# Performance work log

Measured on AMD Instinct MI355X. Metric: run time of the kernel, lower is better.

## Reference

```python
import jax, jax.numpy as jnp
import numpy as np
from jax import lax

EPS = 1e-10
ALPHA = 1000.0

def _gauss_kernel(k=3, mu=0.0, sigma=3.0):
    g1 = np.linspace(-1.0, 1.0, k)
    x, y = np.meshgrid(g1, g1)
    d = np.sqrt(x ** 2 + y ** 2)
    g = np.exp(-(d - mu) ** 2 / (2.0 * sigma ** 2)) / (2.0 * np.pi * sigma ** 2)
    return jnp.asarray(g / g.sum(), jnp.float32)

def _sobel_kernel(k=3, transpose=False):
    r = np.linspace(-(k // 2), k // 2, k)
    x, y = np.meshgrid(r, r)
    den = x ** 2 + y ** 2
    den[:, k // 2] = 1.0
    s = x / den
    if transpose:
        s = s.T
    return jnp.asarray(s, jnp.float32)

def _canny_nms_kernels():
    # 8 directional difference kernels (center minus neighbor), E, SE, S, SW, W, NW, N, NE
    off = [(1, 2), (2, 2), (2, 1), (2, 0), (1, 0), (0, 0), (0, 1), (0, 2)]
    k = np.zeros((8, 3, 3), np.float32)
    k[:, 1, 1] = 1.0
    for i, (r, c) in enumerate(off):
        k[i, r, c] = -1.0
    return jnp.asarray(k)

def _dwconv_reflect(x, k2d):
    # depthwise 3x3 conv with reflect padding (same as padding_mode='reflect', groups=C)
    C = x.shape[1]
    xp = jnp.pad(x, ((0, 0), (0, 0), (1, 1), (1, 1)), mode='reflect')
    w = jnp.broadcast_to(k2d[None, None], (C, 1, 3, 3))
    return lax.conv_general_dilated(xp, w, (1, 1), 'VALID', feature_group_count=C)

def _forward(x, w_expand, w_perm_gauss, w_perm_sx, w_perm_sy, w_merge, low_t, high_t):
    gauss = _gauss_kernel(3, 0.0, 3.0)
    sob_x = _sobel_kernel(3, transpose=False)
    sob_y = _sobel_kernel(3, transpose=True)
    canny = _canny_nms_kernels()  # (8,3,3)
    # 1x1 channel expansion
    h = jnp.einsum('oc,bchw->bohw', w_expand, x)
    # gaussian blur (depthwise) + trainable 1x1 permute
    g = jnp.einsum('oc,bchw->bohw', w_perm_gauss, _dwconv_reflect(h, gauss))
    gx = jnp.einsum('oc,bchw->bohw', w_perm_sx, _dwconv_reflect(g, sob_x))
    gy = jnp.einsum('oc,bchw->bohw', w_perm_sy, _dwconv_reflect(g, sob_y))
    mag = jnp.sqrt(gx * gx + gy * gy + EPS)  # (B,C,H,W)
    # NMSConv2d: every output kernel applies the same directional diff summed over ALL input
    # channels, so the 8C outputs repeat with period 8 -> compute 8 dirs on the channel-sum.
    s = jnp.sum(mag, axis=1, keepdims=True)  # (B,1,H,W)
    dirs = lax.conv_general_dilated(s, canny[:, None], (1, 1), [(1, 1), (1, 1)])  # (B,8,H,W)
    deg = jnp.arctan2(gy, gx) * (180.0 / np.pi)
    idx = jnp.mod(jnp.round(deg / 45.0), 8.0).astype(jnp.int32)  # (B,C,H,W) in [0,8)
    pos = jnp.take_along_axis(dirs[:, None], idx[:, :, None], axis=2)[:, :, 0]
    neg = jnp.take_along_axis(dirs[:, None], ((idx + 4) % 8)[:, :, None], axis=2)[:, :, 0]
    nms = mag * ((pos > 0) & (neg > 0)).astype(mag.dtype)
    # soft double threshold (steep sigmoids)
    strong = jax.nn.sigmoid(ALPHA * (nms - high_t))
    weak = 0.5 * (jax.nn.sigmoid(ALPHA * (high_t - nms)) - jax.nn.sigmoid(ALPHA * (low_t - nms)))
    thr = weak + strong
    # merge C -> 1
    m = jnp.einsum('oc,bchw->bohw', w_merge, thr)  # (B,1,H,W)
    # one-step hysteresis: strong pixels promote neighbouring weak (==0.5) pixels
    img_strong = jnp.where(m == 1.0, m, 0.0)
    masked = (m == 0.5)
    hyst = _dwconv_reflect(img_strong, jnp.full((3, 3), 1.25, m.dtype))
    changed = jnp.where((hyst > 1.0) & masked, m, 0.0) + img_strong
    return changed

def setup_inputs() -> dict:
    key = jax.random.key(0)
    k0, k1, k2 = jax.random.split(key, 3)
    B, Cin, C, H, W = 8, 3, 8, 512, 512
    x = jax.random.uniform(k0, (B, Cin, H, W), jnp.float32)
    w_expand = jax.nn.softmax(jax.random.uniform(k1, (C, Cin), jnp.float32), axis=0)
    eye = jnp.eye(C, dtype=jnp.float32)
    bound = 1.0 / np.sqrt(C)
    w_merge = jax.random.uniform(k2, (1, C), jnp.float32, minval=-bound, maxval=bound)
    low_t = jnp.full((C, 1, 1), 0.1, jnp.float32)
    high_t = jnp.full((C, 1, 1), 0.2, jnp.float32)
    return {'x': x, 'w_expand': w_expand, 'w_perm_gauss': eye, 'w_perm_sx': eye,
            'w_perm_sy': eye, 'w_merge': w_merge, 'low_t': low_t, 'high_t': high_t}

def reference(x, w_expand, w_perm_gauss, w_perm_sx, w_perm_sy, w_merge, low_t, high_t):
    return _forward(x, w_expand, w_perm_gauss, w_perm_sx, w_perm_sy, w_merge, low_t, high_t)
```

## Files before the change

kernel.cpp:

```cpp
#include <hip/hip_runtime.h>
#include <math.h>

#define Bsz 8
#define HWp (512*512)
#define TS 32
#define SG 36
#define MG 34
#define XW 40
#define BW 38
#define NT 512
#define K2E 1442.6950408889634f

#if __has_builtin(__builtin_amdgcn_exp2f)
#define EXP2F(x) __builtin_amdgcn_exp2f(x)
#else
#define EXP2F(x) __expf(0.6931471805599453f*(x))
#endif

__device__ __forceinline__ int refl(int i, int n) {
    i = (i < 0) ? -i : i;
    return (i >= n) ? (2*n - 2 - i) : i;
}

__global__ void k_mats(const float* __restrict__ we, const float* __restrict__ pg,
                       const float* __restrict__ psx, const float* __restrict__ psy,
                       const float* __restrict__ wm, const float* __restrict__ lowt,
                       const float* __restrict__ hight, float* __restrict__ mats) {
    if (threadIdx.x == 0 && blockIdx.x == 0) {
        float M1[8][3];
        for (int o = 0; o < 8; ++o)
            for (int c = 0; c < 3; ++c) {
                float a = 0.f;
                for (int k = 0; k < 8; ++k) a += pg[o*8+k] * we[k*3+c];
                M1[o][c] = a;
            }
        for (int o = 0; o < 8; ++o)
            for (int c = 0; c < 3; ++c) {
                float a = 0.f, b = 0.f;
                for (int k = 0; k < 8; ++k) { a += psx[o*8+k]*M1[k][c]; b += psy[o*8+k]*M1[k][c]; }
                mats[o*3+c]      = a;
                mats[24 + o*3+c] = b;
            }
        for (int o = 0; o < 8; ++o) {
            mats[48+o] = hight[o] * K2E;
            mats[56+o] = lowt[o]  * K2E;
            mats[64+o] = 0.5f * wm[o];
        }
    }
}

__global__ __launch_bounds__(NT) void k_fused(
    const float* __restrict__ x, const float* __restrict__ mats,
    float* __restrict__ out, float wc, float wE, float wk)
{
    __shared__ float sm1[3*XW*XW];
    __shared__ float blb[3*BW*BW];

    const int b  = blockIdx.z;
    const int x0 = blockIdx.x*TS, y0 = blockIdx.y*TS;
    const int t  = threadIdx.x;
    const bool inter = (blockIdx.x > 0) && ((int)blockIdx.x < (int)gridDim.x-1) &&
                       (blockIdx.y > 0) && ((int)blockIdx.y < (int)gridDim.y-1);

    const float* xb = x + (size_t)b*3*HWp;

    if (inter) {
        const float* xo = xb + (size_t)(y0-4)*512 + (x0-4);
        for (int i = t; i < 3*XW*10; i += NT) {
            int c = i/400; int j = i - c*400; int r = j/10; int q = j - r*10;
            float4 v = *(const float4*)(xo + (size_t)c*HWp + r*512 + q*4);
            *(float4*)&sm1[c*(XW*XW) + r*XW + q*4] = v;
        }
    } else {
        for (int i = t; i < XW*XW; i += NT) {
            int r = i/XW, cc = i - r*XW;
            size_t off = (size_t)refl(y0-4+r,512)*512 + refl(x0-4+cc,512);
            #pragma unroll
            for (int c = 0; c < 3; ++c)
                sm1[c*(XW*XW)+i] = xb[(size_t)c*HWp + off];
        }
    }
    __syncthreads();

    if (inter) {
        for (int i = t; i < BW*BW; i += NT) {
            int r = i/BW, cc = i - r*BW;
            const int base = (r+1)*XW + (cc+1);
            #pragma unroll
            for (int c = 0; c < 3; ++c) {
                const float* xp = &sm1[c*(XW*XW) + base];
                blb[c*(BW*BW)+i] =
                    wk*(xp[-XW-1]+xp[-XW+1]+xp[XW-1]+xp[XW+1]) +
                    wE*(xp[-XW]+xp[-1]+xp[1]+xp[XW]) + wc*xp[0];
            }
        }
    } else {
        for (int i = t; i < BW*BW; i += NT) {
            int r = i/BW, cc = i - r*BW;
            int iy = refl(y0-3+r,512) - (y0-4);
            int ix = refl(x0-3+cc,512) - (x0-4);
            const int base = iy*XW + ix;
            #pragma unroll
            for (int c = 0; c < 3; ++c) {
                const float* xp = &sm1[c*(XW*XW) + base];
                blb[c*(BW*BW)+i] =
                    wk*(xp[-XW-1]+xp[-XW+1]+xp[XW-1]+xp[XW+1]) +
                    wE*(xp[-XW]+xp[-1]+xp[1]+xp[XW]) + wc*xp[0];
            }
        }
    }
    __syncthreads();

    float mg[3][8];
    unsigned qk[3];
    #pragma unroll
    for (int it = 0; it < 3; ++it) {
        int i = t + it*NT;
        qk[it] = 0;
        if (i < SG*SG) {
            int r = i/SG, cc = i - r*SG;
            float txv[3], tyv[3];
            #pragma unroll
            for (int c = 0; c < 3; ++c) {
                const float* bp = &blb[c*(BW*BW) + r*BW + cc];
                float v00=bp[0],    v01=bp[1],      v02=bp[2];
                float v10=bp[BW],                   v12=bp[BW+2];
                float v20=bp[2*BW], v21=bp[2*BW+1], v22=bp[2*BW+2];
                txv[c] = 0.5f*(v02-v00) + (v12-v10) + 0.5f*(v22-v20);
                tyv[c] = 0.5f*(v20-v00) + (v21-v01) + 0.5f*(v22-v02);
            }
            float s = 0.f; unsigned pk = 0;
            #pragma unroll
            for (int o = 0; o < 8; ++o) {
                float gx  = mats[o*3]*txv[0]    + mats[o*3+1]*txv[1]    + mats[o*3+2]*txv[2];
                float gy  = mats[24+o*3]*tyv[0] + mats[24+o*3+1]*tyv[1] + mats[24+o*3+2]*tyv[2];
                float mgv = __builtin_amdgcn_sqrtf(gx*gx + gy*gy + 1e-10f);
                mg[it][o] = mgv; s += mgv;
                float ax = fabsf(gx), ay = fabsf(gy);
                unsigned qo;
                if (ay <= 0.41421356237309503f*ax)      qo = 0u;
                else if (ax <= 0.41421356237309503f*ay) qo = 2u;
                else qo = ((gx >= 0.f) == (gy >= 0.f)) ? 1u : 3u;
                pk |= qo << (2*o);
            }
            qk[it] = pk;
            #pragma unroll
            for (int o = 0; o < 8; ++o) { asm volatile("" : "+v"(mg[it][o])); }
            asm volatile("" : "+v"(qk[it]));
            int gy_ = y0-2+r, gx_ = x0-2+cc;
            bool inimg = ((unsigned)gy_ < 512u) && ((unsigned)gx_ < 512u);
            sm1[i] = inimg ? s : 0.f;
        }
    }
    __syncthreads();

    {
        float* sS = sm1;
        float* mS = sm1 + SG*SG;
        const float* hiK = mats + 48;
        const float* loK = mats + 56;
        const float* wmh = mats + 64;
        #pragma unroll
        for (int it = 0; it < 3; ++it) {
            int i = t + it*NT;
            if (i < SG*SG) {
                int r = i/SG, cc = i - r*SG;
                if (r >= 1 && r < SG-1 && cc >= 1 && cc < SG-1) {
                    const float* sp = &sS[i];
                    float sc = sp[0];
                    unsigned mask = 0;
                    mask |= ((sc > sp[1])    && (sc > sp[-1]))    ? 1u : 0u;
                    mask |= ((sc > sp[SG+1]) && (sc > sp[-SG-1])) ? 2u : 0u;
                    mask |= ((sc > sp[SG])   && (sc > sp[-SG]))   ? 4u : 0u;
                    mask |= ((sc > sp[SG-1]) && (sc > sp[-SG+1])) ? 8u : 0u;
                    unsigned pk = qk[it];
                    float m = 0.f;
                    #pragma unroll
                    for (int o = 0; o < 8; ++o) {
                        float nms = ((mask >> ((pk >> (2*o)) & 3u)) & 1u) ? mg[it][o] : 0.f;
                        float shi = __builtin_amdgcn_rcpf(1.f + EXP2F(fmaf(nms, -K2E, hiK[o])));
                        float slo = __builtin_amdgcn_rcpf(1.f + EXP2F(fmaf(nms, -K2E, loK[o])));
                        m += wmh[o]*(shi + slo);
                    }
                    mS[(r-1)*MG + (cc-1)] = m;
                }
            }
        }
    }
    __syncthreads();

    {
        const float* mS = sm1 + SG*SG;
        for (int i2 = t; i2 < TS*TS; i2 += NT) {
            int ty_ = i2/TS, tx_ = i2 - ty_*TS;
            int y = y0 + ty_, xg = x0 + tx_;
            const float* mp = &mS[(ty_+1)*MG + (tx_+1)];
            float mc = mp[0];
            float hy = 0.f;
            if (inter) {
                #pragma unroll
                for (int dy = -1; dy <= 1; ++dy)
                    #pragma unroll
                    for (int dx = -1; dx <= 1; ++dx)
                        hy += (mp[dy*MG+dx] == 1.0f) ? 1.25f : 0.f;
            } else {
                #pragma unroll
                for (int dy = -1; dy <= 1; ++dy)
                    #pragma unroll
                    for (int dx = -1; dx <= 1; ++dx) {
                        int ly = refl(y+dy,512) - (y0-1);
                        int lx = refl(xg+dx,512) - (x0-1);
                        hy += (mS[ly*MG+lx] == 1.0f) ? 1.25f : 0.f;
                    }
            }
            float strong = (mc == 1.0f) ? mc : 0.f;
            out[(size_t)b*HWp + (size_t)y*512 + xg] =
                (((hy > 1.0f) && (mc == 0.5f)) ? mc : 0.f) + strong;
        }
    }
}

extern "C" void kernel_launch(void* const* d_in, const int* in_sizes, int n_in,
                              void* d_out, int out_size, void* d_ws, size_t ws_size,
                              hipStream_t stream) {
    const float* x    = (const float*)d_in[0];
    const float* we   = (const float*)d_in[1];
    const float* pg   = (const float*)d_in[2];
    const float* psx  = (const float*)d_in[3];
    const float* psy  = (const float*)d_in[4];
    const float* wm   = (const float*)d_in[5];
    const float* lowt = (const float*)d_in[6];
    const float* hit  = (const float*)d_in[7];
    float* mats = (float*)d_ws;
    float* outp = (float*)d_out;

    double e1 = exp(-1.0/18.0), e2 = exp(-2.0/18.0);
    double sum = 1.0 + 4.0*e1 + 4.0*e2;
    float wc = (float)(1.0/sum), wE = (float)(e1/sum), wk = (float)(e2/sum);

    k_mats<<<1, 64, 0, stream>>>(we, pg, psx, psy, wm, lowt, hit, mats);
    k_fused<<<dim3(512/TS, 512/TS, Bsz), dim3(NT), 0, stream>>>(
        x, mats, outp, wc, wE, wk);
}
```

Baseline: 53.54 us.

## Use column-strip sliding windows for blur/Sobel and skip tiles without strong pixels

Result: faster. 52.43 us (-2.1%).

```diff
diff --git a/kernel.cpp b/kernel.cpp
--- a/kernel.cpp
+++ b/kernel.cpp
@@ -10,6 +10,7 @@
 #define BW 38
 #define NT 512
 #define K2E 1442.6950408889634f
+#define T2q 0.17157287525380993f
 
 #if __has_builtin(__builtin_amdgcn_exp2f)
 #define EXP2F(x) __builtin_amdgcn_exp2f(x)
@@ -55,12 +56,15 @@
 {
     __shared__ float sm1[3*XW*XW];
     __shared__ float blb[3*BW*BW];
+    __shared__ int anyS;
 
     const int b  = blockIdx.z;
     const int x0 = blockIdx.x*TS, y0 = blockIdx.y*TS;
     const int t  = threadIdx.x;
     const bool inter = (blockIdx.x > 0) && ((int)blockIdx.x < (int)gridDim.x-1) &&
                        (blockIdx.y > 0) && ((int)blockIdx.y < (int)gridDim.y-1);
+
+    if (t == 0) anyS = 0;
 
     const float* xb = x + (size_t)b*3*HWp;
 
@@ -83,15 +87,25 @@
     __syncthreads();
 
     if (inter) {
-        for (int i = t; i < BW*BW; i += NT) {
-            int r = i/BW, cc = i - r*BW;
-            const int base = (r+1)*XW + (cc+1);
-            #pragma unroll
-            for (int c = 0; c < 3; ++c) {
-                const float* xp = &sm1[c*(XW*XW) + base];
-                blb[c*(BW*BW)+i] =
-                    wk*(xp[-XW-1]+xp[-XW+1]+xp[XW-1]+xp[XW+1]) +
-                    wE*(xp[-XW]+xp[-1]+xp[1]+xp[XW]) + wc*xp[0];
+        if (t < 494) {
+            int g = t/38, cb = t - g*38, r0 = 3*g;
+            #pragma unroll
+            for (int c = 0; c < 3; ++c) {
+                const float* col = &sm1[c*(XW*XW) + cb];
+                float* bo = &blb[c*(BW*BW) + cb];
+                float a0 = col[r0*XW],     a1 = col[r0*XW+1],     a2 = col[r0*XW+2];
+                float e0 = col[(r0+1)*XW], e1 = col[(r0+1)*XW+1], e2 = col[(r0+1)*XW+2];
+                #pragma unroll
+                for (int ir = 0; ir < 3; ++ir) {
+                    int r = r0 + ir;
+                    if (r < BW) {
+                        float f0 = col[(r+2)*XW], f1 = col[(r+2)*XW+1], f2 = col[(r+2)*XW+2];
+                        float t0 = a0+f0, t1 = a1+f1, t2 = a2+f2;
+                        float u = t0+t2, v = e0+e2, w = t1+v;
+                        bo[r*BW] = wk*u + wE*w + wc*e1;
+                        a0=e0; a1=e1; a2=e2; e0=f0; e1=f1; e2=f2;
+                    }
+                }
             }
         }
     } else {
@@ -113,76 +127,83 @@
 
     float mg[3][8];
     unsigned qk[3];
-    #pragma unroll
-    for (int it = 0; it < 3; ++it) {
-        int i = t + it*NT;
-        qk[it] = 0;
-        if (i < SG*SG) {
-            int r = i/SG, cc = i - r*SG;
-            float txv[3], tyv[3];
-            #pragma unroll
-            for (int c = 0; c < 3; ++c) {
-                const float* bp = &blb[c*(BW*BW) + r*BW + cc];
-                float v00=bp[0],    v01=bp[1],      v02=bp[2];
-                float v10=bp[BW],                   v12=bp[BW+2];
-                float v20=bp[2*BW], v21=bp[2*BW+1], v22=bp[2*BW+2];
-                txv[c] = 0.5f*(v02-v00) + (v12-v10) + 0.5f*(v22-v20);
-                tyv[c] = 0.5f*(v20-v00) + (v21-v01) + 0.5f*(v22-v02);
-            }
+    const int gC = t/36, csC = t - gC*36, r0C = 3*gC;
+    const bool actC = (t < 432);
+    if (actC) {
+        float txv[3][3], tyv[3][3];
+        #pragma unroll
+        for (int c = 0; c < 3; ++c) {
+            const float* blc = &blb[c*(BW*BW) + csC];
+            float p0 = blc[r0C*BW],     p1 = blc[r0C*BW+1],     p2 = blc[r0C*BW+2];
+            float q0 = blc[(r0C+1)*BW], q1 = blc[(r0C+1)*BW+1], q2 = blc[(r0C+1)*BW+2];
+            float D0 = p2-p0, E0 = fmaf(0.5f, p0+p2, p1);
+            float D1 = q2-q0, E1 = fmaf(0.5f, q0+q2, q1);
+            #pragma unroll
+            for (int ir = 0; ir < 3; ++ir) {
+                const float* wr = &blc[(r0C+2+ir)*BW];
+                float w0 = wr[0], w1 = wr[1], w2 = wr[2];
+                float D2 = w2-w0, E2 = fmaf(0.5f, w0+w2, w1);
+                txv[ir][c] = fmaf(0.5f, D0+D2, D1);
+                tyv[ir][c] = E2 - E0;
+                D0 = D1; D1 = D2; E0 = E1; E1 = E2;
+            }
+        }
+        #pragma unroll
+        for (int ir = 0; ir < 3; ++ir) {
             float s = 0.f; unsigned pk = 0;
             #pragma unroll
             for (int o = 0; o < 8; ++o) {
-                float gx  = mats[o*3]*txv[0]    + mats[o*3+1]*txv[1]    + mats[o*3+2]*txv[2];
-                float gy  = mats[24+o*3]*tyv[0] + mats[24+o*3+1]*tyv[1] + mats[24+o*3+2]*tyv[2];
-                float mgv = __builtin_amdgcn_sqrtf(gx*gx + gy*gy + 1e-10f);
-                mg[it][o] = mgv; s += mgv;
-                float ax = fabsf(gx), ay = fabsf(gy);
-                unsigned qo;
-                if (ay <= 0.41421356237309503f*ax)      qo = 0u;
-                else if (ax <= 0.41421356237309503f*ay) qo = 2u;
-                else qo = ((gx >= 0.f) == (gy >= 0.f)) ? 1u : 3u;
+                float gx = mats[o*3]*txv[ir][0]    + mats[o*3+1]*txv[ir][1]    + mats[o*3+2]*txv[ir][2];
+                float gy = mats[24+o*3]*tyv[ir][0] + mats[24+o*3+1]*tyv[ir][1] + mats[24+o*3+2]*tyv[ir][2];
+                float gx2 = gx*gx, gy2 = gy*gy;
+                float mag = __builtin_amdgcn_sqrtf(gx2 + gy2 + 1e-10f);
+                mg[ir][o] = mag; s += mag;
+                unsigned dv = 1u | (((__float_as_uint(gx) ^ __float_as_uint(gy)) >> 30) & 2u);
+                unsigned qo = (gx2 <= T2q*gy2) ? 2u : dv;
+                qo = (gy2 <= T2q*gx2) ? 0u : qo;
                 pk |= qo << (2*o);
             }
-            qk[it] = pk;
-            #pragma unroll
-            for (int o = 0; o < 8; ++o) { asm volatile("" : "+v"(mg[it][o])); }
-            asm volatile("" : "+v"(qk[it]));
-            int gy_ = y0-2+r, gx_ = x0-2+cc;
+            qk[ir] = pk;
+            #pragma unroll
+            for (int o = 0; o < 8; ++o) { asm volatile("" : "+v"(mg[ir][o])); }
+            asm volatile("" : "+v"(qk[ir]));
+            int rr = r0C + ir;
+            int gy_ = y0-2+rr, gx_ = x0-2+csC;
             bool inimg = ((unsigned)gy_ < 512u) && ((unsigned)gx_ < 512u);
-            sm1[i] = inimg ? s : 0.f;
+            sm1[rr*SG + csC] = inimg ? s : 0.f;
         }
     }
     __syncthreads();
 
     {
-        float* sS = sm1;
+        const float* sS = sm1;
         float* mS = sm1 + SG*SG;
         const float* hiK = mats + 48;
         const float* loK = mats + 56;
         const float* wmh = mats + 64;
-        #pragma unroll
-        for (int it = 0; it < 3; ++it) {
-            int i = t + it*NT;
-            if (i < SG*SG) {
-                int r = i/SG, cc = i - r*SG;
-                if (r >= 1 && r < SG-1 && cc >= 1 && cc < SG-1) {
-                    const float* sp = &sS[i];
+        if (actC && csC >= 1 && csC <= 34) {
+            #pragma unroll
+            for (int ir = 0; ir < 3; ++ir) {
+                int r = r0C + ir;
+                if (r >= 1 && r <= 34) {
+                    const float* sp = &sS[r*SG + csC];
                     float sc = sp[0];
                     unsigned mask = 0;
                     mask |= ((sc > sp[1])    && (sc > sp[-1]))    ? 1u : 0u;
                     mask |= ((sc > sp[SG+1]) && (sc > sp[-SG-1])) ? 2u : 0u;
                     mask |= ((sc > sp[SG])   && (sc > sp[-SG]))   ? 4u : 0u;
                     mask |= ((sc > sp[SG-1]) && (sc > sp[-SG+1])) ? 8u : 0u;
-                    unsigned pk = qk[it];
+                    unsigned pk = qk[ir];
                     float m = 0.f;
                     #pragma unroll
                     for (int o = 0; o < 8; ++o) {
-                        float nms = ((mask >> ((pk >> (2*o)) & 3u)) & 1u) ? mg[it][o] : 0.f;
+                        float nms = ((mask >> ((pk >> (2*o)) & 3u)) & 1u) ? mg[ir][o] : 0.f;
                         float shi = __builtin_amdgcn_rcpf(1.f + EXP2F(fmaf(nms, -K2E, hiK[o])));
                         float slo = __builtin_amdgcn_rcpf(1.f + EXP2F(fmaf(nms, -K2E, loK[o])));
                         m += wmh[o]*(shi + slo);
                     }
-                    mS[(r-1)*MG + (cc-1)] = m;
+                    mS[(r-1)*MG + (csC-1)] = m;
+                    if (m == 1.0f) anyS = 1;
                 }
             }
         }
@@ -191,31 +212,40 @@
 
     {
         const float* mS = sm1 + SG*SG;
-        for (int i2 = t; i2 < TS*TS; i2 += NT) {
-            int ty_ = i2/TS, tx_ = i2 - ty_*TS;
-            int y = y0 + ty_, xg = x0 + tx_;
-            const float* mp = &mS[(ty_+1)*MG + (tx_+1)];
-            float mc = mp[0];
-            float hy = 0.f;
-            if (inter) {
-                #pragma unroll
-                for (int dy = -1; dy <= 1; ++dy)
+        float* op = out + (size_t)b*HWp;
+        if (anyS == 0) {
+            #pragma unroll
+            for (int i2 = t; i2 < TS*TS; i2 += NT) {
+                int ty_ = i2>>5, tx_ = i2&31;
+                op[(size_t)(y0+ty_)*512 + (x0+tx_)] = 0.f;
+            }
+        } else {
+            for (int i2 = t; i2 < TS*TS; i2 += NT) {
+                int ty_ = i2>>5, tx_ = i2&31;
+                int y = y0 + ty_, xg = x0 + tx_;
+                const float* mp = &mS[(ty_+1)*MG + (tx_+1)];
+                float mc = mp[0];
+                float hy = 0.f;
+                if (inter) {
                     #pragma unroll
-                    for (int dx = -1; dx <= 1; ++dx)
-                        hy += (mp[dy*MG+dx] == 1.0f) ? 1.25f : 0.f;
-            } else {
-                #pragma unroll
-                for (int dy = -1; dy <= 1; ++dy)
+                    for (int dy = -1; dy <= 1; ++dy)
+                        #pragma unroll
+                        for (int dx = -1; dx <= 1; ++dx)
+                            hy += (mp[dy*MG+dx] == 1.0f) ? 1.25f : 0.f;
+                } else {
                     #pragma unroll
-                    for (int dx = -1; dx <= 1; ++dx) {
-                        int ly = refl(y+dy,512) - (y0-1);
-                        int lx = refl(xg+dx,512) - (x0-1);
-                        hy += (mS[ly*MG+lx] == 1.0f) ? 1.25f : 0.f;
-                    }
-            }
-            float strong = (mc == 1.0f) ? mc : 0.f;
-            out[(size_t)b*HWp + (size_t)y*512 + xg] =
-                (((hy > 1.0f) && (mc == 0.5f)) ? mc : 0.f) + strong;
+                    for (int dy = -1; dy <= 1; ++dy)
+                        #pragma unroll
+                        for (int dx = -1; dx <= 1; ++dx) {
+                            int ly = refl(y+dy,512) - (y0-1);
+                            int lx = refl(xg+dx,512) - (x0-1);
+                            hy += (mS[ly*MG+lx] == 1.0f) ? 1.25f : 0.f;
+                        }
+                }
+                float strong = (mc == 1.0f) ? mc : 0.f;
+                op[(size_t)y*512 + xg] =
+                    (((hy > 1.0f) && (mc == 0.5f)) ? mc : 0.f) + strong;
+            }
         }
     }
 }
```
